# Performance work log

Hardware: AMD Instinct MI355X
Metric: run time of the kernel (lower is better)

The kernel has to match this reference:

```python
import jax, jax.numpy as jnp
import numpy as np

N_NODES = 100_000
N_EDGES = 1_600_000
N_GRAPHS = 100
NODES_PER_GRAPH = N_NODES // N_GRAPHS
C_IN = 64
C_EDGE = 16
HIDDEN = 64
N_LAYERS = 3
MLP_HIDDEN = 256
N_CLASSES = 4
ENC = 16  # encoding_size; marker column = ENC-1
BN_EPS = 1e-5


def setup_inputs() -> dict:
    key = jax.random.key(0)
    ks = jax.random.split(key, 12)
    spec_idx = jnp.arange(N_GRAPHS, dtype=jnp.int32) * NODES_PER_GRAPH
    x = jax.random.normal(ks[0], (N_NODES, C_IN), jnp.float32)
    # exactly one specified node per graph: x[:, ENC-1] == 1 only at spec_idx
    x = x.at[:, ENC - 1].set(0.0)
    x = x.at[spec_idx, ENC - 1].set(1.0)
    # edges confined within each graph
    eg = jax.random.randint(ks[1], (N_EDGES,), 0, N_GRAPHS)
    src = eg * NODES_PER_GRAPH + jax.random.randint(ks[2], (N_EDGES,), 0, NODES_PER_GRAPH)
    dst = eg * NODES_PER_GRAPH + jax.random.randint(ks[3], (N_EDGES,), 0, NODES_PER_GRAPH)
    edge_index = jnp.stack([src, dst]).astype(jnp.int32)
    edge_attr = jax.random.normal(ks[4], (N_EDGES, C_EDGE), jnp.float32)
    batch = jnp.repeat(jnp.arange(N_GRAPHS, dtype=jnp.int32), NODES_PER_GRAPH)
    neighbor = jax.random.normal(ks[5], (N_GRAPHS, C_IN), jnp.float32)
    msg_in = 2 * HIDDEN + C_EDGE  # 144 (C_IN == HIDDEN)
    s = 1.0 / np.sqrt(msg_in)
    W = jax.random.normal(ks[6], (N_LAYERS, msg_in, HIDDEN), jnp.float32) * s
    b = jax.random.normal(ks[7], (N_LAYERS, HIDDEN), jnp.float32) * s
    bn_gamma = jnp.ones((N_LAYERS, HIDDEN), jnp.float32)
    bn_beta = jnp.zeros((N_LAYERS, HIDDEN), jnp.float32)
    fc1_in = HIDDEN + C_IN + N_LAYERS * HIDDEN  # 320
    fc1_w = jax.random.normal(ks[8], (fc1_in, MLP_HIDDEN), jnp.float32) / np.sqrt(fc1_in)
    fc1_b = jax.random.normal(ks[9], (MLP_HIDDEN,), jnp.float32) / np.sqrt(fc1_in)
    fc2_w = jax.random.normal(ks[10], (MLP_HIDDEN, N_CLASSES), jnp.float32) / np.sqrt(MLP_HIDDEN)
    fc2_b = jax.random.normal(ks[11], (N_CLASSES,), jnp.float32) / np.sqrt(MLP_HIDDEN)
    return {"x": x, "edge_attr": edge_attr, "neighbor": neighbor, "W": W, "b": b,
            "bn_gamma": bn_gamma, "bn_beta": bn_beta, "fc1_w": fc1_w, "fc1_b": fc1_b,
            "fc2_w": fc2_w, "fc2_b": fc2_b, "edge_index": edge_index, "batch": batch,
            "spec_idx": spec_idx}


def reference(x, edge_attr, neighbor, W, b, bn_gamma, bn_beta,
              fc1_w, fc1_b, fc2_w, fc2_b, edge_index, batch, spec_idx):
    N = x.shape[0]
    loops = jnp.arange(N, dtype=edge_index.dtype)
    src = jnp.concatenate([edge_index[0], loops])   # x_j (source)
    dst = jnp.concatenate([edge_index[1], loops])   # x_i (target / aggregate)
    ea = jnp.concatenate([edge_attr, jnp.ones((N, edge_attr.shape[1]), x.dtype)], axis=0)
    bn_scale = 1.0 / jnp.sqrt(jnp.float32(1.0) + BN_EPS)  # eval BN: mean=0, var=1
    embs = []
    for l in range(W.shape[0]):
        # gather -> linear on concat(x_i, x_j, e) -> scatter-add
        m = jnp.concatenate([x[dst], x[src], ea], axis=1) @ W[l] + b[l]  # [E+N, H]
        agg = jax.ops.segment_sum(m, dst, num_segments=N)                # [N, H]
        h = jax.nn.relu(agg)                       # relu inside MP layer
        h = bn_gamma[l] * h * bn_scale + bn_beta[l]  # BatchNorm1d (eval)
        x = jax.nn.relu(h)                         # relu after BN (dropout=eval no-op)
        embs.append(x[spec_idx])
    B = spec_idx.shape[0]
    pooled = jax.ops.segment_sum(x, batch, num_segments=B)  # global_add_pool [B, H]
    feats = jnp.concatenate([pooled] + embs + [neighbor], axis=1)  # [B, 320]
    h = jax.nn.relu(feats @ fc1_w + fc1_b)
    return h @ fc2_w + fc2_b
```

## Files before the change

kernel.cpp:

```cpp
#include <hip/hip_runtime.h>
#include <hip/hip_bf16.h>

#define NN 100000
#define NE 1600000
#define NG 100
#define NPG 1000
#define CE 16
#define HH 64
#define BN_SCALE 0.99999500003749959f
#define NB 512
#define ECH (NE / NB)
#define NBIN 400


typedef __attribute__((ext_vector_type(8))) short bf16x8;
typedef __attribute__((ext_vector_type(4))) float f32x4;
union ABu { bf16x8 f; ushort u[8]; };

__device__ __forceinline__ ushort f2bf_rne(float f) {
  unsigned u = __float_as_uint(f);
  return (ushort)((u + 0x7FFFu + ((u >> 16) & 1u)) >> 16);
}

__global__ __launch_bounds__(256) void k_hist(const int* __restrict__ ei,
                                              int* __restrict__ hist) {
  __shared__ int h[NBIN];
  for (int i = threadIdx.x; i < NBIN; i += 256) h[i] = 0;
  __syncthreads();
  int e0 = blockIdx.x * ECH;
  for (int i = threadIdx.x; i < ECH; i += 256) {
    int d = ei[NE + e0 + i];
    atomicAdd(&h[d / 250], 1);
  }
  __syncthreads();
  for (int i = threadIdx.x; i < NBIN; i += 256) hist[blockIdx.x * NBIN + i] = h[i];
}

__global__ __launch_bounds__(512) void k_scan_a(const int* __restrict__ hist,
                                                int* __restrict__ partial,
                                                int* __restrict__ gtot) {
  __shared__ int sv[512];
  int bin = blockIdx.x, t = threadIdx.x;
  int v = (t < NB) ? hist[t * NBIN + bin] : 0;
  sv[t] = v;
  __syncthreads();
  for (int o = 1; o < 512; o <<= 1) {
    int a = (t >= o) ? sv[t - o] : 0;
    __syncthreads();
    sv[t] += a;
    __syncthreads();
  }
  if (t < NB) partial[t * NBIN + bin] = sv[t] - v;
  if (t == 511) gtot[bin] = sv[511];
}

__global__ __launch_bounds__(512) void k_scan_b(const int* __restrict__ gtot,
                                                int* __restrict__ gbase) {
  __shared__ int sv[512];
  int t = threadIdx.x;
  int v = (t < NBIN) ? gtot[t] : 0;
  sv[t] = v;
  __syncthreads();
  for (int o = 1; o < 512; o <<= 1) {
    int a = (t >= o) ? sv[t - o] : 0;
    __syncthreads();
    sv[t] += a;
    __syncthreads();
  }
  if (t < NBIN) gbase[t] = sv[t] - v;
  if (t == 511) gbase[NBIN] = sv[511];
}

__global__ __launch_bounds__(256) void k_bfill(const int* __restrict__ ei,
                                               const int* __restrict__ partial,
                                               const int* __restrict__ gbase,
                                               unsigned long long* __restrict__ ebuf) {
  __shared__ int cur[NBIN];
  int b = blockIdx.x;
  for (int i = threadIdx.x; i < NBIN; i += 256)
    cur[i] = gbase[i] + partial[b * NBIN + i];
  __syncthreads();
  int e0 = b * ECH;
  for (int i = threadIdx.x; i < ECH; i += 256) {
    int e = e0 + i;
    int d = ei[NE + e], s = ei[e];
    int bin = d / 250;
    int gb = (bin >> 2) * 1000;
    unsigned long long pk = (unsigned long long)(unsigned)e << 32 |
                            (unsigned)((d - gb) << 10) | (unsigned)(s - gb);
    int pos = atomicAdd(&cur[bin], 1);
    ebuf[pos] = pk;
  }
}

__global__ __launch_bounds__(1024) void k_nsort(
    const unsigned long long* __restrict__ ebuf, const int* __restrict__ gbase,
    unsigned* __restrict__ ebuf2, int* __restrict__ rowptr,
    int* __restrict__ cnt) {
  __shared__ int h[250];
  __shared__ int cur[250];
  __shared__ int sv[256];
  int bin = blockIdx.x, t = threadIdx.x;
  int nb = bin * 250, lbase = (bin & 3) * 250;
  int lo = gbase[bin], hi = gbase[bin + 1];
  if (t < 250) h[t] = 0;
  __syncthreads();
  for (int i = lo + t; i < hi; i += 1024) {
    int dl = (int)((ebuf[i] >> 10) & 1023);
    atomicAdd(&h[dl - lbase], 1);
  }
  __syncthreads();
  int v = (t < 250) ? h[t] : 0;
  if (t < 256) sv[t] = v;
  __syncthreads();
  for (int o = 1; o < 256; o <<= 1) {
    int a = (t < 256 && t >= o) ? sv[t - o] : 0;
    __syncthreads();
    if (t < 256) sv[t] += a;
    __syncthreads();
  }
  if (t < 250) {
    int base = lo + sv[t] - v;
    rowptr[nb + t] = base;
    cur[t] = base;
    cnt[nb + t] = v;
  }
  if (bin == NBIN - 1 && t == 0) rowptr[NN] = hi;
  __syncthreads();
  for (int i = lo + t; i < hi; i += 1024) {
    unsigned long long u = ebuf[i];
    int dl = (int)((u >> 10) & 1023);
    unsigned pk = (unsigned)(u >> 32) << 10 | (unsigned)(u & 1023);
    int pos = atomicAdd(&cur[dl - lbase], 1);
    ebuf2[pos] = pk;
  }
}

#define SEB 25000
__global__ __launch_bounds__(256) void k_se3(const unsigned* __restrict__ ebuf2,
                                             const int* __restrict__ rowptr,
                                             const float* __restrict__ ea,
                                             ushort* __restrict__ Se16) {
  int lane = threadIdx.x & 63;
  int slot = lane >> 2;
  int q = lane & 3;
  int orig = blockIdx.x;
  int blk = (orig & 7) * (SEB / 8) + (orig >> 3);
  int n0 = blk * 4 + (threadIdx.x >> 6);
  if (n0 >= NN) return;
  int n = __builtin_amdgcn_readfirstlane(n0);
  int lo = rowptr[n], hi = rowptr[n + 1];
  float aA0 = 0.f, aA1 = 0.f, aA2 = 0.f, aA3 = 0.f;
  float aB0 = 0.f, aB1 = 0.f, aB2 = 0.f, aB3 = 0.f;
  for (int k0 = lo; k0 < hi; k0 += 32) {
    int ka = k0 + slot, kb = k0 + 16 + slot;
    int kca = min(ka, NE - 1), kcb = min(kb, NE - 1);
    unsigned eida = ebuf2[kca] >> 10;
    unsigned eidb = ebuf2[kcb] >> 10;
    float4 va = *(const float4*)(ea + (size_t)eida * CE + q * 4);
    float4 vb = *(const float4*)(ea + (size_t)eidb * CE + q * 4);
    bool oka = ka < hi, okb = kb < hi;
    aA0 += oka ? va.x : 0.f;
    aA1 += oka ? va.y : 0.f;
    aA2 += oka ? va.z : 0.f;
    aA3 += oka ? va.w : 0.f;
    aB0 += okb ? vb.x : 0.f;
    aB1 += okb ? vb.y : 0.f;
    aB2 += okb ? vb.z : 0.f;
    aB3 += okb ? vb.w : 0.f;
  }
  float r0 = aA0 + aB0, r1 = aA1 + aB1, r2 = aA2 + aB2, r3 = aA3 + aB3;
#pragma unroll
  for (int o = 4; o < 64; o <<= 1) {
    r0 += __shfl_xor(r0, o);
    r1 += __shfl_xor(r1, o);
    r2 += __shfl_xor(r2, o);
    r3 += __shfl_xor(r3, o);
  }
  if (lane < 4) {
    unsigned lo32 = (unsigned)f2bf_rne(r0) | ((unsigned)f2bf_rne(r1) << 16);
    unsigned hi32 = (unsigned)f2bf_rne(r2) | ((unsigned)f2bf_rne(r3) << 16);
    *(uint2*)(Se16 + (size_t)n * 16 + lane * 4) = make_uint2(lo32, hi32);
  }
}

#define GEMM_TILES (NN / 16)
#define GB 512
template <typename T>
__global__ __attribute__((amdgpu_waves_per_eu(2, 4))) __launch_bounds__(256)
void k_gemm(const T* __restrict__ x, const float* __restrict__ W,
            const float* __restrict__ b, const int* __restrict__ cnt,
            const ushort* __restrict__ Se16, ushort* __restrict__ y,
            ushort* __restrict__ z) {
  int lane = threadIdx.x & 63;
  int g = lane >> 4, r16 = lane & 15;

  ABu Bm[8][2];
  ABu Bs[4];
  float bias4[4];
#pragma unroll
  for (int t = 0; t < 8; ++t) {
    int col = t * 16 + r16;
    const float* wbase = W + (col < 64 ? 0 : 64 * 64);
    int c64 = col & 63;
#pragma unroll
    for (int h = 0; h < 2; ++h)
#pragma unroll
      for (int e = 0; e < 8; ++e) {
        int k = h * 32 + (e < 4 ? 0 : 16) + 4 * g + (e & 3);
        Bm[t][h].u[e] = f2bf_rne(wbase[k * 64 + c64]);
      }
  }
#pragma unroll
  for (int t = 0; t < 4; ++t) {
    int col = t * 16 + r16;
    float ws = 0.f;
#pragma unroll
    for (int m = 0; m < 16; ++m) ws += W[(128 + m) * 64 + col];
#pragma unroll
    for (int e = 0; e < 8; ++e) {
      int k = (e < 4 ? 0 : 16) + 4 * g + (e & 3);
      float v = (k < 16) ? W[(128 + k) * 64 + col] : (k == 16 ? ws : 0.f);
      Bs[t].u[e] = f2bf_rne(v);
    }
    bias4[t] = b[col];
  }

  int wid = (blockIdx.x << 2) + (threadIdx.x >> 6);
  int nw = GB * 4;
  for (int tt = wid; tt < GEMM_TILES; tt += nw) {
    int nb = tt * 16;
    ABu A0, A1, AS;
    if constexpr (sizeof(T) == 4) {
      const float* xr = (const float*)x + (size_t)(nb + r16) * HH;
      float4 f0 = *(const float4*)(xr + 4 * g);
      float4 f1 = *(const float4*)(xr + 16 + 4 * g);
      float4 f2 = *(const float4*)(xr + 32 + 4 * g);
      float4 f3 = *(const float4*)(xr + 48 + 4 * g);
      A0.u[0] = f2bf_rne(f0.x); A0.u[1] = f2bf_rne(f0.y);
      A0.u[2] = f2bf_rne(f0.z); A0.u[3] = f2bf_rne(f0.w);
      A0.u[4] = f2bf_rne(f1.x); A0.u[5] = f2bf_rne(f1.y);
      A0.u[6] = f2bf_rne(f1.z); A0.u[7] = f2bf_rne(f1.w);
      A1.u[0] = f2bf_rne(f2.x); A1.u[1] = f2bf_rne(f2.y);
      A1.u[2] = f2bf_rne(f2.z); A1.u[3] = f2bf_rne(f2.w);
      A1.u[4] = f2bf_rne(f3.x); A1.u[5] = f2bf_rne(f3.y);
      A1.u[6] = f2bf_rne(f3.z); A1.u[7] = f2bf_rne(f3.w);
    } else {
      const ushort* xr = (const ushort*)x + (size_t)(nb + r16) * HH;
      *(ushort4*)&A0.u[0] = *(const ushort4*)(xr + 4 * g);
      *(ushort4*)&A0.u[4] = *(const ushort4*)(xr + 16 + 4 * g);
      *(ushort4*)&A1.u[0] = *(const ushort4*)(xr + 32 + 4 * g);
      *(ushort4*)&A1.u[4] = *(const ushort4*)(xr + 48 + 4 * g);
    }
    const ushort* sr = Se16 + (size_t)(nb + r16) * 16;
    *(ushort4*)&AS.u[0] = *(const ushort4*)(sr + 4 * g);
    AS.u[4] = (g == 0) ? (ushort)0x3F80 : (ushort)0;
    AS.u[5] = 0; AS.u[6] = 0; AS.u[7] = 0;
    float dq[4];
#pragma unroll
    for (int q = 0; q < 4; ++q) dq[q] = (float)(cnt[nb + 4 * g + q] + 1);

    f32x4 accM[8], accS[4];
#pragma unroll
    for (int t = 0; t < 8; ++t) {
      f32x4 zz = {0.f, 0.f, 0.f, 0.f};
      zz = __builtin_amdgcn_mfma_f32_16x16x32_bf16(A0.f, Bm[t][0].f, zz, 0, 0, 0);
      accM[t] = __builtin_amdgcn_mfma_f32_16x16x32_bf16(A1.f, Bm[t][1].f, zz, 0, 0, 0);
    }
#pragma unroll
    for (int t = 0; t < 4; ++t) {
      f32x4 zz = {0.f, 0.f, 0.f, 0.f};
      accS[t] = __builtin_amdgcn_mfma_f32_16x16x32_bf16(AS.f, Bs[t].f, zz, 0, 0, 0);
    }
#pragma unroll
    for (int q = 0; q < 4; ++q) {
      size_t node = (size_t)(nb + 4 * g + q);
      ushort* zp = z + node * 64 + r16;
      ushort* yp = y + node * 64 + r16;
#pragma unroll
      for (int t = 0; t < 4; ++t) {
        float zv = dq[q] * (accM[t][q] + bias4[t]) + accS[t][q];
        zp[t * 16] = f2bf_rne(zv);
        yp[t * 16] = f2bf_rne(accM[4 + t][q]);
      }
    }
  }
}

#define GTB 25000
__global__ __launch_bounds__(256) void k_gath3(
    const __hip_bfloat16* __restrict__ y, const __hip_bfloat16* __restrict__ z,
    const unsigned* __restrict__ ebuf2, const int* __restrict__ rowptr,
    const float* __restrict__ gamma, const float* __restrict__ beta,
    __hip_bfloat16* __restrict__ xn, float* __restrict__ emb) {
  int lane = threadIdx.x & 63;
  int orig = blockIdx.x;
  int blk = (orig & 7) * (GTB / 8) + (orig >> 3);
  int n0 = blk * 4 + (threadIdx.x >> 6);
  if (n0 >= NN) return;
  int n = __builtin_amdgcn_readfirstlane(n0);
  int lo = rowptr[n], hi = rowptr[n + 1];
  int deg = hi - lo;
  int gb = (n / NPG) * NPG;
  const __hip_bfloat16* yg = y + (size_t)gb * HH;
  float acc = __bfloat162float(z[(size_t)n * HH + lane]) +
              __bfloat162float(y[(size_t)n * HH + lane]);
  int kend = hi - 1;
  for (int k = 0; k < deg; k += 8) {
    int k0 = lo + k;
    int i0 = min(k0 + 0, kend), i1 = min(k0 + 1, kend);
    int i2 = min(k0 + 2, kend), i3 = min(k0 + 3, kend);
    int i4 = min(k0 + 4, kend), i5 = min(k0 + 5, kend);
    int i6 = min(k0 + 6, kend), i7 = min(k0 + 7, kend);
    int s0 = ebuf2[i0] & 1023, s1 = ebuf2[i1] & 1023;
    int s2 = ebuf2[i2] & 1023, s3 = ebuf2[i3] & 1023;
    int s4 = ebuf2[i4] & 1023, s5 = ebuf2[i5] & 1023;
    int s6 = ebuf2[i6] & 1023, s7 = ebuf2[i7] & 1023;
    float v0 = __bfloat162float(yg[(size_t)s0 * HH + lane]);
    float v1 = __bfloat162float(yg[(size_t)s1 * HH + lane]);
    float v2 = __bfloat162float(yg[(size_t)s2 * HH + lane]);
    float v3 = __bfloat162float(yg[(size_t)s3 * HH + lane]);
    float v4 = __bfloat162float(yg[(size_t)s4 * HH + lane]);
    float v5 = __bfloat162float(yg[(size_t)s5 * HH + lane]);
    float v6 = __bfloat162float(yg[(size_t)s6 * HH + lane]);
    float v7 = __bfloat162float(yg[(size_t)s7 * HH + lane]);
    bool o0 = k + 0 < deg, o1 = k + 1 < deg, o2 = k + 2 < deg, o3 = k + 3 < deg;
    bool o4 = k + 4 < deg, o5 = k + 5 < deg, o6 = k + 6 < deg, o7 = k + 7 < deg;
    acc += ((o0 ? v0 : 0.f) + (o1 ? v1 : 0.f)) + ((o2 ? v2 : 0.f) + (o3 ? v3 : 0.f));
    acc += ((o4 ? v4 : 0.f) + (o5 ? v5 : 0.f)) + ((o6 ? v6 : 0.f) + (o7 ? v7 : 0.f));
  }
  acc = fmaxf(acc, 0.f);
  acc = gamma[lane] * acc * BN_SCALE + beta[lane];
  acc = fmaxf(acc, 0.f);
  xn[(size_t)n * HH + lane] = __float2bfloat16(acc);
  if (n % NPG == 0) emb[(n / NPG) * HH + lane] = acc;
}

__global__ __launch_bounds__(512) void k_pool(const __hip_bfloat16* __restrict__ xf,
                                              float* __restrict__ partial) {
  __shared__ float pp[8][64];
  int bin = blockIdx.x;
  int lane = threadIdx.x & 63, wv = threadIdx.x >> 6;
  const __hip_bfloat16* base = xf + (size_t)bin * 250 * HH;
  float acc = 0.f;
  int i = wv;
  for (; i + 24 < 250; i += 32) {
    float v0 = __bfloat162float(base[(size_t)i * HH + lane]);
    float v1 = __bfloat162float(base[(size_t)(i + 8) * HH + lane]);
    float v2 = __bfloat162float(base[(size_t)(i + 16) * HH + lane]);
    float v3 = __bfloat162float(base[(size_t)(i + 24) * HH + lane]);
    acc += (v0 + v1) + (v2 + v3);
  }
  for (; i < 250; i += 8) acc += __bfloat162float(base[(size_t)i * HH + lane]);
  pp[wv][lane] = acc;
  __syncthreads();
  if (wv == 0) {
    float s = ((pp[0][lane] + pp[1][lane]) + (pp[2][lane] + pp[3][lane])) +
              ((pp[4][lane] + pp[5][lane]) + (pp[6][lane] + pp[7][lane]));
    partial[bin * 64 + lane] = s;
  }
}

__global__ __launch_bounds__(256) void k_final(
    const float* __restrict__ partial, const float* __restrict__ emb,
    const float* __restrict__ nbr, const float* __restrict__ fc1w,
    const float* __restrict__ fc1b, const float* __restrict__ fc2w,
    const float* __restrict__ fc2b, float* __restrict__ out) {
  __shared__ float feats[320];
  __shared__ float r1[256];
  __shared__ float red[4][4];
  int g = blockIdx.x;
  int t = threadIdx.x;
  if (t < 64) {
    const float* pb = partial + 4 * g * 64;
    feats[t] = (pb[t] + pb[64 + t]) + (pb[128 + t] + pb[192 + t]);
    feats[256 + t] = nbr[(size_t)g * HH + t];
  } else {
    int j = t - 64;
    feats[64 + j] = emb[((size_t)(j >> 6) * NG + g) * HH + (j & 63)];
  }
  __syncthreads();
  float a0 = fc1b[t], a1 = 0.f, a2 = 0.f, a3 = 0.f;
  const float* wp = fc1w + t;
  for (int k = 0; k < 320; k += 8) {
    float w0 = wp[(k + 0) * 256], w1 = wp[(k + 1) * 256];
    float w2 = wp[(k + 2) * 256], w3 = wp[(k + 3) * 256];
    float w4 = wp[(k + 4) * 256], w5 = wp[(k + 5) * 256];
    float w6 = wp[(k + 6) * 256], w7 = wp[(k + 7) * 256];
    a0 = fmaf(feats[k], w0, a0);
    a1 = fmaf(feats[k + 1], w1, a1);
    a2 = fmaf(feats[k + 2], w2, a2);
    a3 = fmaf(feats[k + 3], w3, a3);
    a0 = fmaf(feats[k + 4], w4, a0);
    a1 = fmaf(feats[k + 5], w5, a1);
    a2 = fmaf(feats[k + 6], w6, a2);
    a3 = fmaf(feats[k + 7], w7, a3);
  }
  float rv = fmaxf((a0 + a1) + (a2 + a3), 0.f);
  r1[t] = rv;
  float p0 = rv * fc2w[t * 4 + 0];
  float p1 = rv * fc2w[t * 4 + 1];
  float p2 = rv * fc2w[t * 4 + 2];
  float p3 = rv * fc2w[t * 4 + 3];
#pragma unroll
  for (int o = 1; o < 64; o <<= 1) {
    p0 += __shfl_xor(p0, o);
    p1 += __shfl_xor(p1, o);
    p2 += __shfl_xor(p2, o);
    p3 += __shfl_xor(p3, o);
  }
  if ((t & 63) == 0) {
    int wv = t >> 6;
    red[wv][0] = p0; red[wv][1] = p1; red[wv][2] = p2; red[wv][3] = p3;
  }
  __syncthreads();
  if (t < 4)
    out[g * 4 + t] = fc2b[t] +
                     ((red[0][t] + red[1][t]) + (red[2][t] + red[3][t]));
}

extern "C" void kernel_launch(void* const* d_in, const int* in_sizes, int n_in,
                              void* d_out, int out_size, void* d_ws, size_t ws_size,
                              hipStream_t stream) {
  const float* x     = (const float*)d_in[0];
  const float* eattr = (const float*)d_in[1];
  const float* nbr   = (const float*)d_in[2];
  const float* W     = (const float*)d_in[3];
  const float* b     = (const float*)d_in[4];
  const float* gamma = (const float*)d_in[5];
  const float* beta  = (const float*)d_in[6];
  const float* fc1w  = (const float*)d_in[7];
  const float* fc1b  = (const float*)d_in[8];
  const float* fc2w  = (const float*)d_in[9];
  const float* fc2b  = (const float*)d_in[10];
  const int*   ei    = (const int*)d_in[11];
  float* out = (float*)d_out;
  (void)in_sizes; (void)n_in; (void)out_size; (void)ws_size;

  char* p = (char*)d_ws;
  size_t off = 0;
  auto alloc = [&](size_t bytes) {
    char* q = p + off;
    off += (bytes + 255) & ~(size_t)255;
    return q;
  };
  int* hist    = (int*)alloc((size_t)NB * NBIN * 4);
  int* partial = (int*)alloc((size_t)NB * NBIN * 4);
  int* gtot    = (int*)alloc((size_t)NBIN * 4);
  int* gbase   = (int*)alloc((size_t)(NBIN + 1) * 4);
  unsigned long long* ebuf = (unsigned long long*)alloc((size_t)NE * 8);
  unsigned* ebuf2 = (unsigned*)alloc((size_t)NE * 4);
  int* rowptr  = (int*)alloc((size_t)(NN + 1) * 4);
  ushort* Se16 = (ushort*)alloc((size_t)NN * 16 * 2);
  int*   cnt   = (int*)alloc((size_t)NN * 4);
  ushort* ybuf = (ushort*)alloc((size_t)NN * HH * 2);
  ushort* zbuf = (ushort*)alloc((size_t)NN * HH * 2);
  ushort* xA   = (ushort*)alloc((size_t)NN * HH * 2);
  ushort* xB   = (ushort*)alloc((size_t)NN * HH * 2);
  float* emb   = (float*)alloc((size_t)3 * NG * HH * 4);
  float* pool  = (float*)alloc((size_t)NBIN * HH * 4);

  k_hist<<<NB, 256, 0, stream>>>(ei, hist);
  k_scan_a<<<NBIN, 512, 0, stream>>>(hist, partial, gtot);
  k_scan_b<<<1, 512, 0, stream>>>(gtot, gbase);
  k_bfill<<<NB, 256, 0, stream>>>(ei, partial, gbase, ebuf);
  k_nsort<<<NBIN, 1024, 0, stream>>>(ebuf, gbase, ebuf2, rowptr, cnt);
  k_se3<<<SEB, 256, 0, stream>>>(ebuf2, rowptr, eattr, Se16);

  k_gemm<float><<<GB, 256, 0, stream>>>(x, W, b, cnt, Se16, ybuf, zbuf);
  k_gath3<<<GTB, 256, 0, stream>>>((const __hip_bfloat16*)ybuf,
                                   (const __hip_bfloat16*)zbuf, ebuf2, rowptr,
                                   gamma, beta, (__hip_bfloat16*)xA, emb);
  k_gemm<ushort><<<GB, 256, 0, stream>>>(xA, W + 144 * 64, b + 64, cnt, Se16,
                                         ybuf, zbuf);
  k_gath3<<<GTB, 256, 0, stream>>>((const __hip_bfloat16*)ybuf,
                                   (const __hip_bfloat16*)zbuf, ebuf2, rowptr,
                                   gamma + 64, beta + 64, (__hip_bfloat16*)xB,
                                   emb + NG * HH);
  k_gemm<ushort><<<GB, 256, 0, stream>>>(xB, W + 2 * 144 * 64, b + 128, cnt,
                                         Se16, ybuf, zbuf);
  k_gath3<<<GTB, 256, 0, stream>>>((const __hip_bfloat16*)ybuf,
                                   (const __hip_bfloat16*)zbuf, ebuf2, rowptr,
                                   gamma + 128, beta + 128, (__hip_bfloat16*)xA,
                                   emb + 2 * NG * HH);

  k_pool<<<NBIN, 512, 0, stream>>>((const __hip_bfloat16*)xA, pool);
  k_final<<<NG, 256, 0, stream>>>(pool, emb, nbr, fc1w, fc1b, fc2w, fc2b, out);
}
```

Measured before the change: 291.1 us.

## Fuse scan kernels, edge-attr sum into sort, and pooling into final MLP

Merges the second scan into the first using a last-block atomic counter. Folds the per-node edge-attribute sum into the node-sort kernel through shared-memory float atomics, which removes the separate k_se3 pass and its second gather over sorted edges. Pooling is fused into the final MLP kernel, now 1024 threads with a split-K fc1. The gather loop drops its clamped, masked tail for an exact remainder loop. This cuts kernel launches and memory passes, at the cost of heavy LDS atomic contention and a non-deterministic float summation order.

```diff
diff --git a/kernel.cpp b/kernel.cpp
--- a/kernel.cpp
+++ b/kernel.cpp
@@ -23,8 +23,10 @@
 }
 
 __global__ __launch_bounds__(256) void k_hist(const int* __restrict__ ei,
-                                              int* __restrict__ hist) {
+                                              int* __restrict__ hist,
+                                              int* __restrict__ gtot) {
   __shared__ int h[NBIN];
+  if (blockIdx.x == 0 && threadIdx.x == 0) gtot[NBIN] = 0;
   for (int i = threadIdx.x; i < NBIN; i += 256) h[i] = 0;
   __syncthreads();
   int e0 = blockIdx.x * ECH;
@@ -38,8 +40,10 @@
 
 __global__ __launch_bounds__(512) void k_scan_a(const int* __restrict__ hist,
                                                 int* __restrict__ partial,
-                                                int* __restrict__ gtot) {
+                                                int* __restrict__ gtot,
+                                                int* __restrict__ gbase) {
   __shared__ int sv[512];
+  __shared__ int last;
   int bin = blockIdx.x, t = threadIdx.x;
   int v = (t < NB) ? hist[t * NBIN + bin] : 0;
   sv[t] = v;
@@ -52,14 +56,13 @@
   }
   if (t < NB) partial[t * NBIN + bin] = sv[t] - v;
   if (t == 511) gtot[bin] = sv[511];
-}
-
-__global__ __launch_bounds__(512) void k_scan_b(const int* __restrict__ gtot,
-                                                int* __restrict__ gbase) {
-  __shared__ int sv[512];
-  int t = threadIdx.x;
-  int v = (t < NBIN) ? gtot[t] : 0;
-  sv[t] = v;
+  __threadfence();
+  __syncthreads();
+  if (t == 0) last = (atomicAdd(&gtot[NBIN], 1) == NBIN - 1) ? 1 : 0;
+  __syncthreads();
+  if (!last) return;
+  int v2 = (t < NBIN) ? gtot[t] : 0;
+  sv[t] = v2;
   __syncthreads();
   for (int o = 1; o < 512; o <<= 1) {
     int a = (t >= o) ? sv[t - o] : 0;
@@ -67,7 +70,7 @@
     sv[t] += a;
     __syncthreads();
   }
-  if (t < NBIN) gbase[t] = sv[t] - v;
+  if (t < NBIN) gbase[t] = sv[t] - v2;
   if (t == 511) gbase[NBIN] = sv[511];
 }
 
@@ -95,8 +98,10 @@
 
 __global__ __launch_bounds__(1024) void k_nsort(
     const unsigned long long* __restrict__ ebuf, const int* __restrict__ gbase,
-    unsigned* __restrict__ ebuf2, int* __restrict__ rowptr,
-    int* __restrict__ cnt) {
+    const float* __restrict__ ea, unsigned* __restrict__ ebuf2,
+    int* __restrict__ rowptr, int* __restrict__ cnt,
+    ushort* __restrict__ Se16) {
+  __shared__ float se[250 * 17];
   __shared__ int h[250];
   __shared__ int cur[250];
   __shared__ int sv[256];
@@ -104,6 +109,7 @@
   int nb = bin * 250, lbase = (bin & 3) * 250;
   int lo = gbase[bin], hi = gbase[bin + 1];
   if (t < 250) h[t] = 0;
+  for (int i = t; i < 250 * 17; i += 1024) se[i] = 0.f;
   __syncthreads();
   for (int i = lo + t; i < hi; i += 1024) {
     int dl = (int)((ebuf[i] >> 10) & 1023);
@@ -129,58 +135,30 @@
   __syncthreads();
   for (int i = lo + t; i < hi; i += 1024) {
     unsigned long long u = ebuf[i];
-    int dl = (int)((u >> 10) & 1023);
+    int dl = (int)((u >> 10) & 1023) - lbase;
     unsigned pk = (unsigned)(u >> 32) << 10 | (unsigned)(u & 1023);
-    int pos = atomicAdd(&cur[dl - lbase], 1);
+    int pos = atomicAdd(&cur[dl], 1);
     ebuf2[pos] = pk;
-  }
-}
-
-#define SEB 25000
-__global__ __launch_bounds__(256) void k_se3(const unsigned* __restrict__ ebuf2,
-                                             const int* __restrict__ rowptr,
-                                             const float* __restrict__ ea,
-                                             ushort* __restrict__ Se16) {
-  int lane = threadIdx.x & 63;
-  int slot = lane >> 2;
-  int q = lane & 3;
-  int orig = blockIdx.x;
-  int blk = (orig & 7) * (SEB / 8) + (orig >> 3);
-  int n0 = blk * 4 + (threadIdx.x >> 6);
-  if (n0 >= NN) return;
-  int n = __builtin_amdgcn_readfirstlane(n0);
-  int lo = rowptr[n], hi = rowptr[n + 1];
-  float aA0 = 0.f, aA1 = 0.f, aA2 = 0.f, aA3 = 0.f;
-  float aB0 = 0.f, aB1 = 0.f, aB2 = 0.f, aB3 = 0.f;
-  for (int k0 = lo; k0 < hi; k0 += 32) {
-    int ka = k0 + slot, kb = k0 + 16 + slot;
-    int kca = min(ka, NE - 1), kcb = min(kb, NE - 1);
-    unsigned eida = ebuf2[kca] >> 10;
-    unsigned eidb = ebuf2[kcb] >> 10;
-    float4 va = *(const float4*)(ea + (size_t)eida * CE + q * 4);
-    float4 vb = *(const float4*)(ea + (size_t)eidb * CE + q * 4);
-    bool oka = ka < hi, okb = kb < hi;
-    aA0 += oka ? va.x : 0.f;
-    aA1 += oka ? va.y : 0.f;
-    aA2 += oka ? va.z : 0.f;
-    aA3 += oka ? va.w : 0.f;
-    aB0 += okb ? vb.x : 0.f;
-    aB1 += okb ? vb.y : 0.f;
-    aB2 += okb ? vb.z : 0.f;
-    aB3 += okb ? vb.w : 0.f;
-  }
-  float r0 = aA0 + aB0, r1 = aA1 + aB1, r2 = aA2 + aB2, r3 = aA3 + aB3;
-#pragma unroll
-  for (int o = 4; o < 64; o <<= 1) {
-    r0 += __shfl_xor(r0, o);
-    r1 += __shfl_xor(r1, o);
-    r2 += __shfl_xor(r2, o);
-    r3 += __shfl_xor(r3, o);
-  }
-  if (lane < 4) {
-    unsigned lo32 = (unsigned)f2bf_rne(r0) | ((unsigned)f2bf_rne(r1) << 16);
-    unsigned hi32 = (unsigned)f2bf_rne(r2) | ((unsigned)f2bf_rne(r3) << 16);
-    *(uint2*)(Se16 + (size_t)n * 16 + lane * 4) = make_uint2(lo32, hi32);
+    unsigned eid = (unsigned)(u >> 32);
+    const float4* er = (const float4*)(ea + (size_t)eid * CE);
+    float4 e0 = er[0], e1 = er[1], e2 = er[2], e3 = er[3];
+    float* sp = &se[dl * 17];
+    atomicAdd(sp + 0, e0.x);  atomicAdd(sp + 1, e0.y);
+    atomicAdd(sp + 2, e0.z);  atomicAdd(sp + 3, e0.w);
+    atomicAdd(sp + 4, e1.x);  atomicAdd(sp + 5, e1.y);
+    atomicAdd(sp + 6, e1.z);  atomicAdd(sp + 7, e1.w);
+    atomicAdd(sp + 8, e2.x);  atomicAdd(sp + 9, e2.y);
+    atomicAdd(sp + 10, e2.z); atomicAdd(sp + 11, e2.w);
+    atomicAdd(sp + 12, e3.x); atomicAdd(sp + 13, e3.y);
+    atomicAdd(sp + 14, e3.z); atomicAdd(sp + 15, e3.w);
+  }
+  __syncthreads();
+  if (t < 1000) {
+    int dl = t >> 2, cg = t & 3;
+    const float* sp = &se[dl * 17 + cg * 4];
+    unsigned lo32 = (unsigned)f2bf_rne(sp[0]) | ((unsigned)f2bf_rne(sp[1]) << 16);
+    unsigned hi32 = (unsigned)f2bf_rne(sp[2]) | ((unsigned)f2bf_rne(sp[3]) << 16);
+    *(uint2*)(Se16 + (size_t)(nb + dl) * 16 + cg * 4) = make_uint2(lo32, hi32);
   }
 }
 
@@ -302,20 +280,16 @@
   int lo = rowptr[n], hi = rowptr[n + 1];
   int deg = hi - lo;
   int gb = (n / NPG) * NPG;
+  const unsigned* cl = ebuf2 + lo;
   const __hip_bfloat16* yg = y + (size_t)gb * HH;
   float acc = __bfloat162float(z[(size_t)n * HH + lane]) +
               __bfloat162float(y[(size_t)n * HH + lane]);
-  int kend = hi - 1;
-  for (int k = 0; k < deg; k += 8) {
-    int k0 = lo + k;
-    int i0 = min(k0 + 0, kend), i1 = min(k0 + 1, kend);
-    int i2 = min(k0 + 2, kend), i3 = min(k0 + 3, kend);
-    int i4 = min(k0 + 4, kend), i5 = min(k0 + 5, kend);
-    int i6 = min(k0 + 6, kend), i7 = min(k0 + 7, kend);
-    int s0 = ebuf2[i0] & 1023, s1 = ebuf2[i1] & 1023;
-    int s2 = ebuf2[i2] & 1023, s3 = ebuf2[i3] & 1023;
-    int s4 = ebuf2[i4] & 1023, s5 = ebuf2[i5] & 1023;
-    int s6 = ebuf2[i6] & 1023, s7 = ebuf2[i7] & 1023;
+  int k = 0;
+  for (; k + 8 <= deg; k += 8) {
+    int s0 = cl[k] & 1023, s1 = cl[k + 1] & 1023;
+    int s2 = cl[k + 2] & 1023, s3 = cl[k + 3] & 1023;
+    int s4 = cl[k + 4] & 1023, s5 = cl[k + 5] & 1023;
+    int s6 = cl[k + 6] & 1023, s7 = cl[k + 7] & 1023;
     float v0 = __bfloat162float(yg[(size_t)s0 * HH + lane]);
     float v1 = __bfloat162float(yg[(size_t)s1 * HH + lane]);
     float v2 = __bfloat162float(yg[(size_t)s2 * HH + lane]);
@@ -324,11 +298,10 @@
     float v5 = __bfloat162float(yg[(size_t)s5 * HH + lane]);
     float v6 = __bfloat162float(yg[(size_t)s6 * HH + lane]);
     float v7 = __bfloat162float(yg[(size_t)s7 * HH + lane]);
-    bool o0 = k + 0 < deg, o1 = k + 1 < deg, o2 = k + 2 < deg, o3 = k + 3 < deg;
-    bool o4 = k + 4 < deg, o5 = k + 5 < deg, o6 = k + 6 < deg, o7 = k + 7 < deg;
-    acc += ((o0 ? v0 : 0.f) + (o1 ? v1 : 0.f)) + ((o2 ? v2 : 0.f) + (o3 ? v3 : 0.f));
-    acc += ((o4 ? v4 : 0.f) + (o5 ? v5 : 0.f)) + ((o6 ? v6 : 0.f) + (o7 ? v7 : 0.f));
-  }
+    acc += ((v0 + v1) + (v2 + v3)) + ((v4 + v5) + (v6 + v7));
+  }
+  for (; k < deg; ++k)
+    acc += __bfloat162float(yg[(size_t)(cl[k] & 1023) * HH + lane]);
   acc = fmaxf(acc, 0.f);
   acc = gamma[lane] * acc * BN_SCALE + beta[lane];
   acc = fmaxf(acc, 0.f);
@@ -336,53 +309,49 @@
   if (n % NPG == 0) emb[(n / NPG) * HH + lane] = acc;
 }
 
-__global__ __launch_bounds__(512) void k_pool(const __hip_bfloat16* __restrict__ xf,
-                                              float* __restrict__ partial) {
-  __shared__ float pp[8][64];
-  int bin = blockIdx.x;
-  int lane = threadIdx.x & 63, wv = threadIdx.x >> 6;
-  const __hip_bfloat16* base = xf + (size_t)bin * 250 * HH;
-  float acc = 0.f;
-  int i = wv;
-  for (; i + 24 < 250; i += 32) {
-    float v0 = __bfloat162float(base[(size_t)i * HH + lane]);
-    float v1 = __bfloat162float(base[(size_t)(i + 8) * HH + lane]);
-    float v2 = __bfloat162float(base[(size_t)(i + 16) * HH + lane]);
-    float v3 = __bfloat162float(base[(size_t)(i + 24) * HH + lane]);
-    acc += (v0 + v1) + (v2 + v3);
-  }
-  for (; i < 250; i += 8) acc += __bfloat162float(base[(size_t)i * HH + lane]);
-  pp[wv][lane] = acc;
-  __syncthreads();
-  if (wv == 0) {
-    float s = ((pp[0][lane] + pp[1][lane]) + (pp[2][lane] + pp[3][lane])) +
-              ((pp[4][lane] + pp[5][lane]) + (pp[6][lane] + pp[7][lane]));
-    partial[bin * 64 + lane] = s;
-  }
-}
-
-__global__ __launch_bounds__(256) void k_final(
-    const float* __restrict__ partial, const float* __restrict__ emb,
+__global__ __launch_bounds__(1024) void k_final(
+    const __hip_bfloat16* __restrict__ xf, const float* __restrict__ emb,
     const float* __restrict__ nbr, const float* __restrict__ fc1w,
     const float* __restrict__ fc1b, const float* __restrict__ fc2w,
     const float* __restrict__ fc2b, float* __restrict__ out) {
+  __shared__ float pp[16][64];
   __shared__ float feats[320];
-  __shared__ float r1[256];
+  __shared__ float r1p[4][256];
   __shared__ float red[4][4];
   int g = blockIdx.x;
   int t = threadIdx.x;
+  int lane = t & 63, wv = t >> 6;
+  const __hip_bfloat16* base = xf + (size_t)g * NPG * HH;
+  float acc = 0.f;
+  int i = wv;
+  for (; i + 48 < NPG; i += 64) {
+    float v0 = __bfloat162float(base[(size_t)i * HH + lane]);
+    float v1 = __bfloat162float(base[(size_t)(i + 16) * HH + lane]);
+    float v2 = __bfloat162float(base[(size_t)(i + 32) * HH + lane]);
+    float v3 = __bfloat162float(base[(size_t)(i + 48) * HH + lane]);
+    acc += (v0 + v1) + (v2 + v3);
+  }
+  for (; i < NPG; i += 16) acc += __bfloat162float(base[(size_t)i * HH + lane]);
+  pp[wv][lane] = acc;
+  __syncthreads();
   if (t < 64) {
-    const float* pb = partial + 4 * g * 64;
-    feats[t] = (pb[t] + pb[64 + t]) + (pb[128 + t] + pb[192 + t]);
+    float s = 0.f;
+#pragma unroll
+    for (int w = 0; w < 16; ++w) s += pp[w][t];
+    feats[t] = s;
     feats[256 + t] = nbr[(size_t)g * HH + t];
-  } else {
+  } else if (t < 256) {
     int j = t - 64;
     feats[64 + j] = emb[((size_t)(j >> 6) * NG + g) * HH + (j & 63)];
-  }
-  __syncthreads();
-  float a0 = fc1b[t], a1 = 0.f, a2 = 0.f, a3 = 0.f;
-  const float* wp = fc1w + t;
-  for (int k = 0; k < 320; k += 8) {
+  } else if (t < 384) {
+    int j = t - 256 + 128;
+    feats[64 + j] = emb[((size_t)(j >> 6) * NG + g) * HH + (j & 63)];
+  }
+  __syncthreads();
+  int o = t & 255, tg = t >> 8;
+  float a0 = 0.f, a1 = 0.f, a2 = 0.f, a3 = 0.f;
+  const float* wp = fc1w + o;
+  for (int k = tg * 80; k < tg * 80 + 80; k += 8) {
     float w0 = wp[(k + 0) * 256], w1 = wp[(k + 1) * 256];
     float w2 = wp[(k + 2) * 256], w3 = wp[(k + 3) * 256];
     float w4 = wp[(k + 4) * 256], w5 = wp[(k + 5) * 256];
@@ -396,22 +365,26 @@
     a2 = fmaf(feats[k + 6], w6, a2);
     a3 = fmaf(feats[k + 7], w7, a3);
   }
-  float rv = fmaxf((a0 + a1) + (a2 + a3), 0.f);
-  r1[t] = rv;
-  float p0 = rv * fc2w[t * 4 + 0];
-  float p1 = rv * fc2w[t * 4 + 1];
-  float p2 = rv * fc2w[t * 4 + 2];
-  float p3 = rv * fc2w[t * 4 + 3];
-#pragma unroll
-  for (int o = 1; o < 64; o <<= 1) {
-    p0 += __shfl_xor(p0, o);
-    p1 += __shfl_xor(p1, o);
-    p2 += __shfl_xor(p2, o);
-    p3 += __shfl_xor(p3, o);
-  }
-  if ((t & 63) == 0) {
-    int wv = t >> 6;
-    red[wv][0] = p0; red[wv][1] = p1; red[wv][2] = p2; red[wv][3] = p3;
+  r1p[tg][o] = (a0 + a1) + (a2 + a3);
+  __syncthreads();
+  if (t < 256) {
+    float rv = fmaxf(fc1b[t] + ((r1p[0][t] + r1p[1][t]) + (r1p[2][t] + r1p[3][t])),
+                     0.f);
+    float p0 = rv * fc2w[t * 4 + 0];
+    float p1 = rv * fc2w[t * 4 + 1];
+    float p2 = rv * fc2w[t * 4 + 2];
+    float p3 = rv * fc2w[t * 4 + 3];
+#pragma unroll
+    for (int oo = 1; oo < 64; oo <<= 1) {
+      p0 += __shfl_xor(p0, oo);
+      p1 += __shfl_xor(p1, oo);
+      p2 += __shfl_xor(p2, oo);
+      p3 += __shfl_xor(p3, oo);
+    }
+    if ((t & 63) == 0) {
+      red[t >> 6][0] = p0; red[t >> 6][1] = p1;
+      red[t >> 6][2] = p2; red[t >> 6][3] = p3;
+    }
   }
   __syncthreads();
   if (t < 4)
@@ -446,7 +419,7 @@
   };
   int* hist    = (int*)alloc((size_t)NB * NBIN * 4);
   int* partial = (int*)alloc((size_t)NB * NBIN * 4);
-  int* gtot    = (int*)alloc((size_t)NBIN * 4);
+  int* gtot    = (int*)alloc((size_t)(NBIN + 1) * 4);
   int* gbase   = (int*)alloc((size_t)(NBIN + 1) * 4);
   unsigned long long* ebuf = (unsigned long long*)alloc((size_t)NE * 8);
   unsigned* ebuf2 = (unsigned*)alloc((size_t)NE * 4);
@@ -458,14 +431,11 @@
   ushort* xA   = (ushort*)alloc((size_t)NN * HH * 2);
   ushort* xB   = (ushort*)alloc((size_t)NN * HH * 2);
   float* emb   = (float*)alloc((size_t)3 * NG * HH * 4);
-  float* pool  = (float*)alloc((size_t)NBIN * HH * 4);
-
-  k_hist<<<NB, 256, 0, stream>>>(ei, hist);
-  k_scan_a<<<NBIN, 512, 0, stream>>>(hist, partial, gtot);
-  k_scan_b<<<1, 512, 0, stream>>>(gtot, gbase);
+
+  k_hist<<<NB, 256, 0, stream>>>(ei, hist, gtot);
+  k_scan_a<<<NBIN, 512, 0, stream>>>(hist, partial, gtot, gbase);
   k_bfill<<<NB, 256, 0, stream>>>(ei, partial, gbase, ebuf);
-  k_nsort<<<NBIN, 1024, 0, stream>>>(ebuf, gbase, ebuf2, rowptr, cnt);
-  k_se3<<<SEB, 256, 0, stream>>>(ebuf2, rowptr, eattr, Se16);
+  k_nsort<<<NBIN, 1024, 0, stream>>>(ebuf, gbase, eattr, ebuf2, rowptr, cnt, Se16);
 
   k_gemm<float><<<GB, 256, 0, stream>>>(x, W, b, cnt, Se16, ybuf, zbuf);
   k_gath3<<<GTB, 256, 0, stream>>>((const __hip_bfloat16*)ybuf,
@@ -484,6 +454,6 @@
                                    gamma + 128, beta + 128, (__hip_bfloat16*)xA,
                                    emb + 2 * NG * HH);
 
-  k_pool<<<NBIN, 512, 0, stream>>>((const __hip_bfloat16*)xA, pool);
-  k_final<<<NG, 256, 0, stream>>>(pool, emb, nbr, fc1w, fc1b, fc2w, fc2b, out);
-}
+  k_final<<<NG, 1024, 0, stream>>>((const __hip_bfloat16*)xA, emb, nbr, fc1w,
+                                   fc1b, fc2w, fc2b, out);
+}
```

Measured after the change: 460.1 us. +58.1%, slower.
